# Kernel optimization log

Hardware: AMD Instinct MI355X
Metric: run time of the kernel (lower is better)

The kernel has to match this reference:

```python
import jax, jax.numpy as jnp
import numpy as np

B, V, J = 2, 4, 24
HM = 96          # heatmap H == W
VOL = 48         # volumetric grid side
FOCAL = 80.0
CAM_DIST = 3.0


def _make_proj_matrices():
    # Pinhole cameras orbiting the unit cube, looking at the origin.
    K = np.array([[FOCAL, 0.0, HM / 2.0],
                  [0.0, FOCAL, HM / 2.0],
                  [0.0, 0.0, 1.0]], dtype=np.float32)
    mats = []
    for v in range(V):
        a = 2.0 * np.pi * v / V
        R = np.array([[np.cos(a), 0.0, np.sin(a)],
                      [0.0, 1.0, 0.0],
                      [-np.sin(a), 0.0, np.cos(a)]], dtype=np.float32)
        t = np.array([[0.0], [0.0], [CAM_DIST]], dtype=np.float32)
        mats.append(K @ np.concatenate([R, t], axis=1))  # [3,4]
    return np.stack(mats).astype(np.float32)  # [V,3,4]


def setup_inputs() -> dict:
    key = jax.random.key(0)
    k1, k2 = jax.random.split(key)
    heatmaps = jax.random.uniform(k1, (B, V, J, HM, HM), dtype=jnp.float32)
    # coord volume: [-1,1]^3 grid with a small per-batch jitter
    lin = np.linspace(-1.0, 1.0, VOL, dtype=np.float32)
    grid = np.stack(np.meshgrid(lin, lin, lin, indexing='ij'), axis=-1)  # [VOL,VOL,VOL,3]
    offs = np.asarray(jax.random.uniform(k2, (B, 1, 1, 1, 3), minval=-0.1, maxval=0.1))
    coord_volumes = jnp.asarray(grid[None] + offs, dtype=jnp.float32)  # [B,VOL,VOL,VOL,3]
    proj = np.broadcast_to(_make_proj_matrices()[None], (B, V, 3, 4)).copy()
    proj_matricies = jnp.asarray(proj)
    return {"heatmaps": heatmaps, "proj_matricies": proj_matricies, "coord_volumes": coord_volumes}


def _bilinear_sample(img, ix, iy):
    # img: [J,H,W]; ix,iy: [N] pixel coords, align_corners=True, zero padding
    Hh, Ww = img.shape[1], img.shape[2]
    x0 = jnp.floor(ix)
    y0 = jnp.floor(iy)
    wx1 = ix - x0
    wy1 = iy - y0
    wx0 = 1.0 - wx1
    wy0 = 1.0 - wy1
    x0i = x0.astype(jnp.int32)
    y0i = y0.astype(jnp.int32)
    x1i = x0i + 1
    y1i = y0i + 1

    def gather(yc, xc):
        valid = ((xc >= 0) & (xc < Ww) & (yc >= 0) & (yc < Hh)).astype(img.dtype)
        v = img[:, jnp.clip(yc, 0, Hh - 1), jnp.clip(xc, 0, Ww - 1)]  # [J,N]
        return v * valid[None, :]

    return (wy0 * wx0 * gather(y0i, x0i) + wy0 * wx1 * gather(y0i, x1i)
            + wy1 * wx0 * gather(y1i, x0i) + wy1 * wx1 * gather(y1i, x1i))  # [J,N]


def _forward(heatmaps, proj_matricies, coord_volumes):
    b, v, j, hh, ww = heatmaps.shape
    xs, ys, zs = coord_volumes.shape[1:4]
    n = xs * ys * zs
    grid = coord_volumes.reshape(b, n, 3)
    grid_h = jnp.concatenate([grid, jnp.ones((b, n, 1), grid.dtype)], axis=-1)  # [b,n,4]
    proj = jnp.einsum('bnk,bvjk->bvnj', grid_h, proj_matricies)  # [b,v,n,3] homogeneous
    z = proj[..., 2]
    invalid = z <= 0.0
    z_safe = jnp.where(z == 0.0, jnp.ones_like(z), z)
    px = proj[..., 0] / z_safe
    py = proj[..., 1] / z_safe
    # original normalizes x by heatmap_shape[0] (=H) and y by heatmap_shape[1] (=W)
    gx = 2.0 * (px / hh - 0.5)
    gy = 2.0 * (py / ww - 0.5)
    # grid_sample align_corners=True pixel coords: x indexes W, y indexes H
    ix = (gx + 1.0) * 0.5 * (ww - 1)
    iy = (gy + 1.0) * 0.5 * (hh - 1)
    sample = jax.vmap(jax.vmap(_bilinear_sample))(heatmaps, ix, iy)  # [b,v,j,n]
    sample = jnp.where(invalid[:, :, None, :], jnp.zeros_like(sample), sample)
    volume = sample.sum(axis=1).reshape(b, j, xs, ys, zs)  # 'sum' aggregation
    # integrate_tensor_3d_with_coordinates (softmax=True)
    vol_sm = jax.nn.softmax(volume.reshape(b, j, -1), axis=2).reshape(b, j, xs, ys, zs)
    coordinates = jnp.einsum('bnxyz,bxyzc->bnc', vol_sm, coord_volumes)  # [b,j,3]
    return coordinates


def reference(heatmaps, proj_matricies, coord_volumes):
    return _forward(heatmaps, proj_matricies, coord_volumes)
```

## Files before the change

### kernel.cpp

```cpp
#include <hip/hip_runtime.h>

#define BATCH 2
#define NVIEW 4
#define NJOINT 24
#define HM 96
#define VOLD 48
#define NVOX (VOLD*VOLD*VOLD)
#define IMG (HM*HM)
#define HMT_OFF 256
#define RED_STRIDE 260

__global__ __launch_bounds__(256) void transpose_kernel(
    const float* __restrict__ hm, float* __restrict__ hmT)
{
    const int o  = blockIdx.x * 256 + threadIdx.x;
    const int j  = o % NJOINT;
    const int r  = o / NJOINT;
    const int xy = r % IMG;
    const int bv = r / IMG;
    hmT[o] = hm[(bv * NJOINT + j) * IMG + xy];
}

__global__ __launch_bounds__(256, 2) void vol_main_kernel(
    const float* __restrict__ hmT,
    const float* __restrict__ pm,
    const float* __restrict__ cv,
    float* __restrict__ acc)
{
    __shared__ float Xt[VOLD], Yt[VOLD], Zt[VOLD];
    __shared__ float red[NJOINT * RED_STRIDE];
    __shared__ float red2[NJOINT * 4];

    const int tid = threadIdx.x;
    const int gid = blockIdx.x * 256 + tid;
    const int b   = gid / NVOX;
    const int m   = gid - b * NVOX;
    const int z   = m % VOLD;
    const int t2  = m / VOLD;
    const int y   = t2 % VOLD;
    const int x   = t2 / VOLD;

    const float* cvb = cv + (size_t)b * NVOX * 3;
    if (tid < VOLD) {
        Xt[tid] = cvb[(size_t)tid * (VOLD * VOLD * 3)];
        Yt[tid] = cvb[(size_t)tid * (VOLD * 3) + 1];
        Zt[tid] = cvb[(size_t)tid * 3 + 2];
    }

    float Mv[NVIEW][12];
#pragma unroll
    for (int v = 0; v < NVIEW; ++v)
#pragma unroll
        for (int k = 0; k < 12; ++k) Mv[v][k] = pm[(b * NVIEW + v) * 12 + k];

    __syncthreads();

    const float X = Xt[x], Y = Yt[y], Z = Zt[z];

    float vol[NJOINT];
#pragma unroll
    for (int q = 0; q < NJOINT; ++q) vol[q] = 0.f;

#pragma unroll
    for (int v = 0; v < NVIEW; ++v) {
        const float* mv = Mv[v];
        const float pz  = fmaf(mv[8], X, fmaf(mv[9], Y, fmaf(mv[10], Z, mv[11])));
        const float pxn = fmaf(mv[0], X, fmaf(mv[1], Y, fmaf(mv[2],  Z, mv[3])));
        const float pyn = fmaf(mv[4], X, fmaf(mv[5], Y, fmaf(mv[6],  Z, mv[7])));

        const float pzc = pz > 0.f ? pz : 1.0f;
        const float inv = __builtin_amdgcn_rcpf(pzc) * (95.0f / 96.0f);
        const float ix  = pxn * inv;
        const float iy  = pyn * inv;

        const float x0f = floorf(ix), y0f = floorf(iy);
        const float wx1 = ix - x0f,  wy1 = iy - y0f;
        const int x0 = (int)x0f, y0 = (int)y0f;
        const int x1 = x0 + 1,   y1 = y0 + 1;

        const bool vz = pz > 0.f;
        const float wx0m = ((unsigned)x0 < (unsigned)HM) ? (1.f - wx1) : 0.f;
        const float wx1m = ((unsigned)x1 < (unsigned)HM) ? wx1 : 0.f;
        const float wy0m = (((unsigned)y0 < (unsigned)HM) && vz) ? (1.f - wy1) : 0.f;
        const float wy1m = (((unsigned)y1 < (unsigned)HM) && vz) ? wy1 : 0.f;

        const float w00 = wy0m * wx0m, w01 = wy0m * wx1m;
        const float w10 = wy1m * wx0m, w11 = wy1m * wx1m;

        const int xc0 = min(max(x0, 0), HM - 1);
        const int xc1 = min(max(x1, 0), HM - 1);
        const int yc0 = min(max(y0, 0), HM - 1);
        const int yc1 = min(max(y1, 0), HM - 1);

        const float* base = hmT + (size_t)(b * NVIEW + v) * (IMG * NJOINT);
        const float4* p00 = (const float4*)(base + (yc0 * HM + xc0) * NJOINT);
        const float4* p01 = (const float4*)(base + (yc0 * HM + xc1) * NJOINT);
        const float4* p10 = (const float4*)(base + (yc1 * HM + xc0) * NJOINT);
        const float4* p11 = (const float4*)(base + (yc1 * HM + xc1) * NJOINT);

#pragma unroll
        for (int c4 = 0; c4 < 6; ++c4) {
            const float4 f00 = p00[c4];
            const float4 f01 = p01[c4];
            const float4 f10 = p10[c4];
            const float4 f11 = p11[c4];
            vol[c4*4+0] = fmaf(w00, f00.x, fmaf(w01, f01.x, fmaf(w10, f10.x, fmaf(w11, f11.x, vol[c4*4+0]))));
            vol[c4*4+1] = fmaf(w00, f00.y, fmaf(w01, f01.y, fmaf(w10, f10.y, fmaf(w11, f11.y, vol[c4*4+1]))));
            vol[c4*4+2] = fmaf(w00, f00.z, fmaf(w01, f01.z, fmaf(w10, f10.z, fmaf(w11, f11.z, vol[c4*4+2]))));
            vol[c4*4+3] = fmaf(w00, f00.w, fmaf(w01, f01.w, fmaf(w10, f10.w, fmaf(w11, f11.w, vol[c4*4+3]))));
        }
    }

#pragma unroll
    for (int q = 0; q < NJOINT; ++q) vol[q] = __expf(vol[q]);

#pragma unroll
    for (int p = 0; p < 4; ++p) {
        const float scale = (p == 0) ? 1.0f : (p == 1) ? X : (p == 2) ? Y : Z;
#pragma unroll
        for (int q = 0; q < NJOINT; ++q)
            red[q * RED_STRIDE + tid] = vol[q] * scale;
        __syncthreads();

        if (tid < 96) {
            const int q = tid % NJOINT, seg = tid / NJOINT;
            const float4* row = (const float4*)&red[q * RED_STRIDE + seg * 64];
            float s = 0.f;
#pragma unroll
            for (int i = 0; i < 16; ++i) {
                const float4 f = row[i];
                s += (f.x + f.y) + (f.z + f.w);
            }
            red2[seg * NJOINT + q] = s;
        }
        __syncthreads();

        if (tid < NJOINT) {
            const float s = (red2[tid] + red2[tid + 24]) + (red2[tid + 48] + red2[tid + 72]);
            atomicAdd(&acc[(b * NJOINT + tid) * 4 + p], s);
        }
        __syncthreads();
    }
}

__global__ void finalize_kernel(const float* __restrict__ acc, float* __restrict__ out)
{
    const int i = threadIdx.x;
    if (i < BATCH * NJOINT * 3) {
        const int bj = i / 3;
        const int c  = i - bj * 3;
        out[i] = acc[bj * 4 + 1 + c] / acc[bj * 4 + 0];
    }
}

extern "C" void kernel_launch(void* const* d_in, const int* in_sizes, int n_in,
                              void* d_out, int out_size, void* d_ws, size_t ws_size,
                              hipStream_t stream)
{
    const float* hm = (const float*)d_in[0];
    const float* pm = (const float*)d_in[1];
    const float* cv = (const float*)d_in[2];
    float* out = (float*)d_out;
    float* acc = (float*)d_ws;
    float* hmT = (float*)d_ws + HMT_OFF;

    hipMemsetAsync(acc, 0, BATCH * NJOINT * 4 * sizeof(float), stream);

    transpose_kernel<<<(BATCH*NVIEW*NJOINT*IMG)/256, 256, 0, stream>>>(hm, hmT);

    vol_main_kernel<<<(BATCH*NVOX)/256, 256, 0, stream>>>(hmT, pm, cv, acc);

    finalize_kernel<<<1, 192, 0, stream>>>(acc, out);
}
```

Baseline: 145.3 us.

## Split joints across blocks, tile voxels into 4x4x4 bricks, fuse finalize via last-block

Each block now handles half of the joints (12) for a 4x4x4 brick of voxels per wavefront, which halves per-thread register and shared-memory use and allows launch bounds of 8 blocks per SM. Voxel bricks improve gather locality in the heatmap, and blocks are interleaved across the grid. The memset and finalize kernels are removed: the transpose kernel zeroes the accumulators and the counter, and the last block to finish computes the output through an atomic counter. In exchange, the projection and bilinear weight maths is duplicated for each joint group and the number of atomics per output grows.

After: 216.7 us. 1.49x slower.

```diff
diff --git a/kernel.cpp b/kernel.cpp
--- a/kernel.cpp
+++ b/kernel.cpp
@@ -3,16 +3,25 @@
 #define BATCH 2
 #define NVIEW 4
 #define NJOINT 24
+#define JG 12
 #define HM 96
 #define VOLD 48
 #define NVOX (VOLD*VOLD*VOLD)
 #define IMG (HM*HM)
+#define CHUNKS 432
+#define TOTAL_BLOCKS (BATCH*2*CHUNKS)
+#define CNT_OFF 192
 #define HMT_OFF 256
 #define RED_STRIDE 260
 
 __global__ __launch_bounds__(256) void transpose_kernel(
-    const float* __restrict__ hm, float* __restrict__ hmT)
+    const float* __restrict__ hm, float* __restrict__ hmT,
+    float* __restrict__ acc, unsigned* __restrict__ counter)
 {
+    if (blockIdx.x == 0) {
+        if (threadIdx.x < 192) acc[threadIdx.x] = 0.f;
+        if (threadIdx.x == 192) *counter = 0u;
+    }
     const int o  = blockIdx.x * 256 + threadIdx.x;
     const int j  = o % NJOINT;
     const int r  = o / NJOINT;
@@ -21,24 +30,37 @@
     hmT[o] = hm[(bv * NJOINT + j) * IMG + xy];
 }
 
-__global__ __launch_bounds__(256, 2) void vol_main_kernel(
+__global__ __launch_bounds__(256, 8) void vol_main_kernel(
     const float* __restrict__ hmT,
     const float* __restrict__ pm,
     const float* __restrict__ cv,
-    float* __restrict__ acc)
+    float* __restrict__ acc,
+    unsigned* __restrict__ counter,
+    float* __restrict__ out)
 {
     __shared__ float Xt[VOLD], Yt[VOLD], Zt[VOLD];
-    __shared__ float red[NJOINT * RED_STRIDE];
-    __shared__ float red2[NJOINT * 4];
+    __shared__ float red[JG * RED_STRIDE];
+    __shared__ float red2[48];
+    __shared__ int lastFlag;
 
     const int tid = threadIdx.x;
-    const int gid = blockIdx.x * 256 + tid;
-    const int b   = gid / NVOX;
-    const int m   = gid - b * NVOX;
-    const int z   = m % VOLD;
-    const int t2  = m / VOLD;
-    const int y   = t2 % VOLD;
-    const int x   = t2 / VOLD;
+
+    const int logical = (blockIdx.x & 7) * (TOTAL_BLOCKS / 8) + (blockIdx.x >> 3);
+    const int b   = logical / (2 * CHUNKS);
+    const int rem = logical - b * (2 * CHUNKS);
+    const int jg  = rem / CHUNKS;
+    const int c   = rem - jg * CHUNKS;
+
+    const int w    = tid >> 6;
+    const int ln   = tid & 63;
+    const int beta = c * 4 + w;
+    const int bx   = beta / 144;
+    const int r2   = beta - bx * 144;
+    const int by   = r2 / 12;
+    const int bz   = r2 - by * 12;
+    const int x = bx * 4 + (ln >> 4);
+    const int y = by * 4 + ((ln >> 2) & 3);
+    const int z = bz * 4 + (ln & 3);
 
     const float* cvb = cv + (size_t)b * NVOX * 3;
     if (tid < VOLD) {
@@ -57,9 +79,9 @@
 
     const float X = Xt[x], Y = Yt[y], Z = Zt[z];
 
-    float vol[NJOINT];
+    float vol[JG];
 #pragma unroll
-    for (int q = 0; q < NJOINT; ++q) vol[q] = 0.f;
+    for (int q = 0; q < JG; ++q) vol[q] = 0.f;
 
 #pragma unroll
     for (int v = 0; v < NVIEW; ++v) {
@@ -92,14 +114,14 @@
         const int yc0 = min(max(y0, 0), HM - 1);
         const int yc1 = min(max(y1, 0), HM - 1);
 
-        const float* base = hmT + (size_t)(b * NVIEW + v) * (IMG * NJOINT);
+        const float* base = hmT + (size_t)(b * NVIEW + v) * (IMG * NJOINT) + jg * JG;
         const float4* p00 = (const float4*)(base + (yc0 * HM + xc0) * NJOINT);
         const float4* p01 = (const float4*)(base + (yc0 * HM + xc1) * NJOINT);
         const float4* p10 = (const float4*)(base + (yc1 * HM + xc0) * NJOINT);
         const float4* p11 = (const float4*)(base + (yc1 * HM + xc1) * NJOINT);
 
 #pragma unroll
-        for (int c4 = 0; c4 < 6; ++c4) {
+        for (int c4 = 0; c4 < JG / 4; ++c4) {
             const float4 f00 = p00[c4];
             const float4 f01 = p01[c4];
             const float4 f10 = p10[c4];
@@ -112,18 +134,18 @@
     }
 
 #pragma unroll
-    for (int q = 0; q < NJOINT; ++q) vol[q] = __expf(vol[q]);
+    for (int q = 0; q < JG; ++q) vol[q] = __expf(vol[q]);
 
 #pragma unroll
     for (int p = 0; p < 4; ++p) {
         const float scale = (p == 0) ? 1.0f : (p == 1) ? X : (p == 2) ? Y : Z;
 #pragma unroll
-        for (int q = 0; q < NJOINT; ++q)
+        for (int q = 0; q < JG; ++q)
             red[q * RED_STRIDE + tid] = vol[q] * scale;
         __syncthreads();
 
-        if (tid < 96) {
-            const int q = tid % NJOINT, seg = tid / NJOINT;
+        if (tid < 48) {
+            const int q = tid % JG, seg = tid / JG;
             const float4* row = (const float4*)&red[q * RED_STRIDE + seg * 64];
             float s = 0.f;
 #pragma unroll
@@ -131,25 +153,30 @@
                 const float4 f = row[i];
                 s += (f.x + f.y) + (f.z + f.w);
             }
-            red2[seg * NJOINT + q] = s;
+            red2[seg * JG + q] = s;
         }
         __syncthreads();
 
-        if (tid < NJOINT) {
-            const float s = (red2[tid] + red2[tid + 24]) + (red2[tid + 48] + red2[tid + 72]);
-            atomicAdd(&acc[(b * NJOINT + tid) * 4 + p], s);
+        if (tid < JG) {
+            const float s = (red2[tid] + red2[tid + JG]) + (red2[tid + 2*JG] + red2[tid + 3*JG]);
+            atomicAdd(&acc[(b * NJOINT + jg * JG + tid) * 4 + p], s);
         }
         __syncthreads();
     }
-}
 
-__global__ void finalize_kernel(const float* __restrict__ acc, float* __restrict__ out)
-{
-    const int i = threadIdx.x;
-    if (i < BATCH * NJOINT * 3) {
-        const int bj = i / 3;
-        const int c  = i - bj * 3;
-        out[i] = acc[bj * 4 + 1 + c] / acc[bj * 4 + 0];
+    __threadfence();
+    __syncthreads();
+    if (tid == 0) {
+        const unsigned t = atomicAdd(counter, 1u);
+        lastFlag = (t == TOTAL_BLOCKS - 1u);
+    }
+    __syncthreads();
+    if (lastFlag && tid < BATCH * NJOINT * 3) {
+        const int bj = tid / 3;
+        const int cc = tid - bj * 3;
+        const float num = atomicAdd(&acc[bj * 4 + 1 + cc], 0.f);
+        const float den = atomicAdd(&acc[bj * 4 + 0], 0.f);
+        out[tid] = num / den;
     }
 }
 
@@ -162,13 +189,9 @@
     const float* cv = (const float*)d_in[2];
     float* out = (float*)d_out;
     float* acc = (float*)d_ws;
+    unsigned* counter = (unsigned*)d_ws + CNT_OFF;
     float* hmT = (float*)d_ws + HMT_OFF;
 
-    hipMemsetAsync(acc, 0, BATCH * NJOINT * 4 * sizeof(float), stream);
-
-    transpose_kernel<<<(BATCH*NVIEW*NJOINT*IMG)/256, 256, 0, stream>>>(hm, hmT);
-
-    vol_main_kernel<<<(BATCH*NVOX)/256, 256, 0, stream>>>(hmT, pm, cv, acc);
-
-    finalize_kernel<<<1, 192, 0, stream>>>(acc, out);
+    transpose_kernel<<<(BATCH*NVIEW*NJOINT*IMG)/256, 256, 0, stream>>>(hm, hmT, acc, counter);
+    vol_main_kernel<<<TOTAL_BLOCKS, 256, 0, stream>>>(hmT, pm, cv, acc, counter, out);
 }
```
